# Kernel optimization log

Hardware: AMD Instinct MI355X
Metric: run time of the kernel (lower is better)

## Reference

```python
import jax, jax.numpy as jnp
import numpy as np

N = 100000   # nodes (single ntype)
R = 3        # relations
E = 500000   # edges per relation
H = 4        # attention heads
F = 64       # out_feat per head
IN = 256     # in_feat
NEG_SLOPE = 0.2  # DGL GATConv default


def setup_inputs() -> dict:
    key = jax.random.key(0)
    ks = jax.random.split(key, 7)
    x = jax.random.normal(ks[0], (N, IN), jnp.float32)
    src = jax.random.randint(ks[1], (R, E), 0, N, dtype=jnp.int32)
    dst = jax.random.randint(ks[2], (R, E), 0, N, dtype=jnp.int32)
    W = jax.random.normal(ks[3], (R, IN, H * F), jnp.float32) / np.sqrt(IN).astype(np.float32)
    attn_l = jax.random.normal(ks[4], (R, H, F), jnp.float32) * 0.1
    attn_r = jax.random.normal(ks[5], (R, H, F), jnp.float32) * 0.1
    bias = jnp.zeros((R, H * F), jnp.float32)
    return {"x": x, "W": W, "attn_l": attn_l, "attn_r": attn_r, "bias": bias,
            "src": src, "dst": dst}


def _gat_relation(x, W_r, al_r, ar_r, b_r, src_r, dst_r):
    # projection: [N, H, F]
    z = (x @ W_r).reshape(N, H, F)
    # per-node attention logits: [N, H]
    el = jnp.sum(z * al_r, axis=-1)
    er = jnp.sum(z * ar_r, axis=-1)
    # edge scores: [E, H]
    e = jax.nn.leaky_relu(el[src_r] + er[dst_r], negative_slope=NEG_SLOPE)
    # segment softmax over incoming edges of each dst node
    m = jax.ops.segment_max(e, dst_r, num_segments=N)      # [N, H]
    ee = jnp.exp(e - m[dst_r])                              # [E, H]
    den = jax.ops.segment_sum(ee, dst_r, num_segments=N)   # [N, H]
    alpha = ee / den[dst_r]                                 # [E, H]
    # weighted scatter-aggregate: [N, H, F]
    rst = jax.ops.segment_sum(z[src_r] * alpha[:, :, None], dst_r, num_segments=N)
    return rst + b_r.reshape(1, H, F)


def reference(x, W, attn_l, attn_r, bias, src, dst):
    # HeteroGraphConv aggregates relations targeting the same ntype with 'sum'
    out = jnp.zeros((N, H, F), x.dtype)
    for r in range(R):
        out = out + _gat_relation(x, W[r], attn_l[r], attn_r[r], bias[r], src[r], dst[r])
    # RelGATConvLayer._apply: activation(h.view(-1, out_feat*num_heads)); dropout=0
    return jax.nn.elu(out.reshape(N, H * F))
```

## Files before the change

### kernel.cpp

```cpp
#include <hip/hip_runtime.h>
#include <hip/hip_bf16.h>


#define RN 100000
#define RE 500000
#define RH 4
#define RIN 256
#define RR 3
#define RHF 256
#define NE3 (RR * RE)

typedef __attribute__((ext_vector_type(8))) short short8;
typedef __attribute__((ext_vector_type(4))) float f32x4;

static __device__ __forceinline__ float b2f(unsigned short u) {
  return __uint_as_float(((unsigned int)u) << 16);
}
static __device__ __forceinline__ unsigned short f2b(float f) {
  unsigned int u = __float_as_uint(f);
  u += 0x7FFF + ((u >> 16) & 1);
  return (unsigned short)(u >> 16);
}

__global__ __launch_bounds__(256) void rgat_convx(
    const float* __restrict__ x, unsigned short* __restrict__ xb) {
  const size_t i = ((size_t)blockIdx.x * 256 + threadIdx.x) * 4;
  if (i >= (size_t)RN * RIN) return;
  const float4 v = *(const float4*)(x + i);
  ushort4 o;
  o.x = f2b(v.x); o.y = f2b(v.y); o.z = f2b(v.z); o.w = f2b(v.w);
  *(ushort4*)(xb + i) = o;
}

__global__ __launch_bounds__(256) void rgat_convw(
    const float* __restrict__ W, unsigned short* __restrict__ wbt) {
  const int o = blockIdx.x * 256 + threadIdx.x;
  if (o >= RR * RIN * RHF) return;
  const int r = o / (RIN * RHF);
  const int rem = o - r * (RIN * RHF);
  const int n = rem >> 8;
  const int k = rem & 255;
  wbt[o] = f2b(W[r * (RIN * RHF) + k * RHF + n]);
}

__global__ __launch_bounds__(256) void rgat_gemm_bf16(
    const unsigned short* __restrict__ xb, const unsigned short* __restrict__ wbt,
    unsigned short* __restrict__ zb, const float* __restrict__ al,
    const float* __restrict__ ar, float* __restrict__ el,
    float* __restrict__ er) {
  __shared__ unsigned short As[128 * 32];
  __shared__ unsigned short Bs[128 * 32];
  const int tid = threadIdx.x;
  const int lane = tid & 63, wid = tid >> 6;
  const int wr = wid >> 1, wc = wid & 1;
  const int m0 = blockIdx.x * 128;
  const int n0 = blockIdx.y * 128;
  const int r  = blockIdx.z;

  f32x4 acc[4][4] = {};
  const unsigned short* Bbase = wbt + (size_t)r * (RIN * RHF);

  for (int k0 = 0; k0 < RIN; k0 += 32) {
#pragma unroll
    for (int i = 0; i < 2; ++i) {
      const int c = wid * 128 + i * 64 + lane;
      const int row = c >> 2, c4 = c & 3;
      const unsigned short* ga = xb + (size_t)(m0 + row) * RIN + k0 + c4 * 8;
      __builtin_amdgcn_global_load_lds(
          (const __attribute__((address_space(1))) void*)ga,
          (__attribute__((address_space(3))) void*)(As + (wid * 128 + i * 64) * 8),
          16, 0, 0);
      const unsigned short* gb = Bbase + (size_t)(n0 + row) * RIN + k0 + c4 * 8;
      __builtin_amdgcn_global_load_lds(
          (const __attribute__((address_space(1))) void*)gb,
          (__attribute__((address_space(3))) void*)(Bs + (wid * 128 + i * 64) * 8),
          16, 0, 0);
    }
    asm volatile("s_waitcnt vmcnt(0)" ::: "memory");
    __syncthreads();

    short8 af[4], bfr[4];
#pragma unroll
    for (int mi = 0; mi < 4; ++mi)
      af[mi] = *(const short8*)(As + ((wr * 64 + mi * 16 + (lane & 15)) * 32 + (lane >> 4) * 8));
#pragma unroll
    for (int ni = 0; ni < 4; ++ni)
      bfr[ni] = *(const short8*)(Bs + ((wc * 64 + ni * 16 + (lane & 15)) * 32 + (lane >> 4) * 8));
#pragma unroll
    for (int mi = 0; mi < 4; ++mi)
#pragma unroll
      for (int ni = 0; ni < 4; ++ni)
        acc[mi][ni] = __builtin_amdgcn_mfma_f32_16x16x32_bf16(af[mi], bfr[ni], acc[mi][ni], 0, 0, 0);
    __syncthreads();
  }

  const int head = blockIdx.y * 2 + wc;
  float alv[4], arv[4];
#pragma unroll
  for (int ni = 0; ni < 4; ++ni) {
    alv[ni] = al[r * RHF + head * 64 + ni * 16 + (lane & 15)];
    arv[ni] = ar[r * RHF + head * 64 + ni * 16 + (lane & 15)];
  }

  const int mbase = m0 + wr * 64;
#pragma unroll
  for (int mi = 0; mi < 4; ++mi) {
#pragma unroll
    for (int q = 0; q < 4; ++q) {
      const int m = mbase + mi * 16 + (lane >> 4) * 4 + q;
      float pl = 0.f, pr = 0.f;
#pragma unroll
      for (int ni = 0; ni < 4; ++ni) {
        pl += acc[mi][ni][q] * alv[ni];
        pr += acc[mi][ni][q] * arv[ni];
      }
#pragma unroll
      for (int off = 1; off < 16; off <<= 1) {
        pl += __shfl_xor(pl, off);
        pr += __shfl_xor(pr, off);
      }
      if (m < RN) {
        if ((lane & 15) == 0) {
          el[(size_t)(r * (size_t)RN + m) * RH + head] = pl;
          er[(size_t)(r * (size_t)RN + m) * RH + head] = pr;
        }
        unsigned short* zrow = zb + (size_t)r * ((size_t)RN * RHF) + (size_t)m * RHF
                               + n0 + wc * 64 + (lane & 15);
#pragma unroll
        for (int ni = 0; ni < 4; ++ni) zrow[ni * 16] = f2b(acc[mi][ni][q]);
      }
    }
  }
}

__global__ __launch_bounds__(256) void rgat_hist(
    const int* __restrict__ dst, int* __restrict__ degm) {
  const int i = blockIdx.x * 256 + threadIdx.x;
  if (i >= NE3) return;
  atomicAdd(&degm[dst[i]], 1);
}

__global__ __launch_bounds__(256) void rgat_scan1(
    const int* __restrict__ deg, int* __restrict__ offs, int* __restrict__ bsum) {
  __shared__ int sh[256];
  const int tid = threadIdx.x;
  const int base = blockIdx.x * 1024 + tid * 4;
  int v[4]; int s = 0;
#pragma unroll
  for (int j = 0; j < 4; ++j) {
    v[j] = (base + j < RN) ? deg[base + j] : 0;
    s += v[j];
  }
  sh[tid] = s;
  __syncthreads();
  for (int off = 1; off < 256; off <<= 1) {
    int t = (tid >= off) ? sh[tid - off] : 0;
    __syncthreads();
    sh[tid] += t;
    __syncthreads();
  }
  int run = sh[tid] - s;
  if (tid == 255) bsum[blockIdx.x] = sh[255];
#pragma unroll
  for (int j = 0; j < 4; ++j) {
    if (base + j < RN) offs[base + j] = run;
    run += v[j];
  }
}

__global__ __launch_bounds__(512) void rgat_scan2(int* __restrict__ bsum, int nb) {
  __shared__ int sh[512];
  const int tid = threadIdx.x;
  const int v = (tid < nb) ? bsum[tid] : 0;
  sh[tid] = v;
  __syncthreads();
  for (int off = 1; off < 512; off <<= 1) {
    int t = (tid >= off) ? sh[tid - off] : 0;
    __syncthreads();
    sh[tid] += t;
    __syncthreads();
  }
  if (tid < nb) bsum[tid] = sh[tid] - v;
}

__global__ __launch_bounds__(256) void rgat_scan3(
    int* __restrict__ offs, const int* __restrict__ bsum) {
  const int base = blockIdx.x * 1024 + threadIdx.x * 4;
  const int b = bsum[blockIdx.x];
#pragma unroll
  for (int j = 0; j < 4; ++j)
    if (base + j < RN) offs[base + j] += b;
}

__global__ __launch_bounds__(256) void rgat_scatter(
    const int* __restrict__ src, const int* __restrict__ dst,
    const float* __restrict__ el, const float* __restrict__ er,
    int* __restrict__ offsm, int* __restrict__ czoff,
    float4* __restrict__ cee) {
  const int i = blockIdx.x * 256 + threadIdx.x;
  if (i >= NE3) return;
  const int r = i / RE;
  const int s = src[i];
  const int d = dst[i];
  const int pos = atomicAdd(&offsm[d], 1);
  const float4 elv = *(const float4*)(el + (size_t)(r * (size_t)RN + s) * RH);
  const float4 erv = *(const float4*)(er + (size_t)(r * (size_t)RN + d) * RH);
  float e0 = elv.x + erv.x, e1 = elv.y + erv.y, e2 = elv.z + erv.z, e3 = elv.w + erv.w;
  e0 = e0 > 0.f ? e0 : 0.2f * e0;
  e1 = e1 > 0.f ? e1 : 0.2f * e1;
  e2 = e2 > 0.f ? e2 : 0.2f * e2;
  e3 = e3 > 0.f ? e3 : 0.2f * e3;
  czoff[pos] = r * RN + s;
  cee[pos] = make_float4(__expf(e0), __expf(e1), __expf(e2), __expf(e3));
}

__global__ __launch_bounds__(256) void rgat_aggregate(
    const unsigned short* __restrict__ zb, const int* __restrict__ czoff,
    const float4* __restrict__ cee, const int* __restrict__ degm,
    const int* __restrict__ offsm, const float* __restrict__ bias,
    float* __restrict__ out) {
  __shared__ float shn[4][RR][RHF];
  __shared__ float shd[4][RR][RH];
  const int n = blockIdx.x;
  const int wid = threadIdx.x >> 6, lane = threadIdx.x & 63;
  const int h = lane >> 4;
  const int c = lane * 4;

  const int d = degm[n];
  const int start = offsm[n] - d;

  float4 acc0 = {0.f, 0.f, 0.f, 0.f}, acc1 = acc0, acc2 = acc0;
  float den0 = 0.f, den1 = 0.f, den2 = 0.f;

  const unsigned short* zc = zb + c;

  for (int base = wid; base < d; base += 16) {
    int zo[4];
    float4 ef[4];
    ushort4 zv[4];
#pragma unroll
    for (int j = 0; j < 4; ++j) {
      const int t = base + j * 4;
      if (t < d) {
        zo[j] = czoff[start + t];
        ef[j] = cee[start + t];
      } else {
        zo[j] = -1;
      }
    }
#pragma unroll
    for (int j = 0; j < 4; ++j)
      if (zo[j] >= 0) zv[j] = *(const ushort4*)(zc + (size_t)zo[j] * RHF);
#pragma unroll
    for (int j = 0; j < 4; ++j) {
      if (zo[j] < 0) continue;
      const float a = (h == 0) ? ef[j].x : (h == 1) ? ef[j].y : (h == 2) ? ef[j].z : ef[j].w;
      const float z0 = b2f(zv[j].x), z1 = b2f(zv[j].y), z2 = b2f(zv[j].z), z3 = b2f(zv[j].w);
      if (zo[j] < RN) {
        acc0.x += a * z0; acc0.y += a * z1; acc0.z += a * z2; acc0.w += a * z3; den0 += a;
      } else if (zo[j] < 2 * RN) {
        acc1.x += a * z0; acc1.y += a * z1; acc1.z += a * z2; acc1.w += a * z3; den1 += a;
      } else {
        acc2.x += a * z0; acc2.y += a * z1; acc2.z += a * z2; acc2.w += a * z3; den2 += a;
      }
    }
  }

  *(float4*)&shn[wid][0][c] = acc0;
  *(float4*)&shn[wid][1][c] = acc1;
  *(float4*)&shn[wid][2][c] = acc2;
  if ((lane & 15) == 0) {
    shd[wid][0][h] = den0;
    shd[wid][1][h] = den1;
    shd[wid][2][h] = den2;
  }
  __syncthreads();

  const int col = threadIdx.x;
  const int hh = col >> 6;
  float v = bias[col] + bias[RHF + col] + bias[2 * RHF + col];
#pragma unroll
  for (int r = 0; r < RR; ++r) {
    const float dn = shd[0][r][hh] + shd[1][r][hh] + shd[2][r][hh] + shd[3][r][hh];
    const float nm = shn[0][r][col] + shn[1][r][col] + shn[2][r][col] + shn[3][r][col];
    v += (dn > 0.f) ? nm / dn : 0.f;
  }
  v = v > 0.f ? v : (__expf(v) - 1.f);
  out[(size_t)n * RHF + col] = v;
}

extern "C" void kernel_launch(void* const* d_in, const int* in_sizes, int n_in,
                              void* d_out, int out_size, void* d_ws, size_t ws_size,
                              hipStream_t stream) {
  const float* x    = (const float*)d_in[0];
  const float* W    = (const float*)d_in[1];
  const float* al   = (const float*)d_in[2];
  const float* ar   = (const float*)d_in[3];
  const float* bias = (const float*)d_in[4];
  const int*   src  = (const int*)d_in[5];
  const int*   dst  = (const int*)d_in[6];
  float* out = (float*)d_out;

  char* p = (char*)d_ws;
  unsigned short* xb  = (unsigned short*)p; p += (size_t)RN * RIN * 2;
  unsigned short* wbt = (unsigned short*)p; p += (size_t)RR * RIN * RHF * 2;
  unsigned short* zb  = (unsigned short*)p; p += (size_t)RR * RN * RHF * 2;
  float* el    = (float*)p;  p += (size_t)RR * RN * RH * 4;
  float* er    = (float*)p;  p += (size_t)RR * RN * RH * 4;
  int* degm    = (int*)p;    p += (size_t)RN * 4;
  int* offsm   = (int*)p;    p += (size_t)RN * 4;
  int* czoff   = (int*)p;    p += (size_t)NE3 * 4;
  float4* cee  = (float4*)p; p += (size_t)NE3 * 16;
  int* bsum    = (int*)p;    p += 2048;

  const int NB1 = (RN + 1023) / 1024;

  hipMemsetAsync(degm, 0, (size_t)RN * 4, stream);

  rgat_convx<<<(RN * RIN / 4 + 255) / 256, 256, 0, stream>>>(x, xb);
  rgat_convw<<<(RR * RIN * RHF + 255) / 256, 256, 0, stream>>>(W, wbt);

  rgat_hist<<<(NE3 + 255) / 256, 256, 0, stream>>>(dst, degm);
  rgat_scan1<<<NB1, 256, 0, stream>>>(degm, offsm, bsum);
  rgat_scan2<<<1, 512, 0, stream>>>(bsum, NB1);
  rgat_scan3<<<NB1, 256, 0, stream>>>(offsm, bsum);

  rgat_gemm_bf16<<<dim3((RN + 127) / 128, RHF / 128, RR), 256, 0, stream>>>(
      xb, wbt, zb, al, ar, el, er);

  rgat_scatter<<<(NE3 + 255) / 256, 256, 0, stream>>>(src, dst, el, er, offsm,
                                                      czoff, cee);

  rgat_aggregate<<<RN, 256, 0, stream>>>(zb, czoff, cee, degm, offsm, bias, out);
}
```

Before: 646.5 us.

## Bucket CSR edges by (dst, relation) and gather 8-wide bf16 rows per half-wave

The CSR is now keyed by (dst node, relation), so the degree histogram, scan and scatter run over N*R buckets instead of N. The aggregate kernel loops per relation without per-edge branches and stores only the source index. Each half-wave handles one edge and loads 16-byte short8 rows, which doubles the gather width per lane. The scan now covers three times as many entries (294 scan blocks, within the 512-thread scan2 limit), and the aggregate loop has less unrolled memory-level parallelism.

```diff
diff --git a/kernel.cpp b/kernel.cpp
--- a/kernel.cpp
+++ b/kernel.cpp
@@ -9,6 +9,7 @@
 #define RR 3
 #define RHF 256
 #define NE3 (RR * RE)
+#define N3  (RR * RN)
 
 typedef __attribute__((ext_vector_type(8))) short short8;
 typedef __attribute__((ext_vector_type(4))) float f32x4;
@@ -134,10 +135,11 @@
 }
 
 __global__ __launch_bounds__(256) void rgat_hist(
-    const int* __restrict__ dst, int* __restrict__ degm) {
+    const int* __restrict__ dst, int* __restrict__ deg2) {
   const int i = blockIdx.x * 256 + threadIdx.x;
   if (i >= NE3) return;
-  atomicAdd(&degm[dst[i]], 1);
+  const int r = i / RE;
+  atomicAdd(&deg2[dst[i] * RR + r], 1);
 }
 
 __global__ __launch_bounds__(256) void rgat_scan1(
@@ -148,7 +150,7 @@
   int v[4]; int s = 0;
 #pragma unroll
   for (int j = 0; j < 4; ++j) {
-    v[j] = (base + j < RN) ? deg[base + j] : 0;
+    v[j] = (base + j < N3) ? deg[base + j] : 0;
     s += v[j];
   }
   sh[tid] = s;
@@ -163,7 +165,7 @@
   if (tid == 255) bsum[blockIdx.x] = sh[255];
 #pragma unroll
   for (int j = 0; j < 4; ++j) {
-    if (base + j < RN) offs[base + j] = run;
+    if (base + j < N3) offs[base + j] = run;
     run += v[j];
   }
 }
@@ -189,20 +191,20 @@
   const int b = bsum[blockIdx.x];
 #pragma unroll
   for (int j = 0; j < 4; ++j)
-    if (base + j < RN) offs[base + j] += b;
+    if (base + j < N3) offs[base + j] += b;
 }
 
 __global__ __launch_bounds__(256) void rgat_scatter(
     const int* __restrict__ src, const int* __restrict__ dst,
     const float* __restrict__ el, const float* __restrict__ er,
-    int* __restrict__ offsm, int* __restrict__ czoff,
+    int* __restrict__ offs2, int* __restrict__ csrc,
     float4* __restrict__ cee) {
   const int i = blockIdx.x * 256 + threadIdx.x;
   if (i >= NE3) return;
   const int r = i / RE;
   const int s = src[i];
   const int d = dst[i];
-  const int pos = atomicAdd(&offsm[d], 1);
+  const int pos = atomicAdd(&offs2[d * RR + r], 1);
   const float4 elv = *(const float4*)(el + (size_t)(r * (size_t)RN + s) * RH);
   const float4 erv = *(const float4*)(er + (size_t)(r * (size_t)RN + d) * RH);
   float e0 = elv.x + erv.x, e1 = elv.y + erv.y, e2 = elv.z + erv.z, e3 = elv.w + erv.w;
@@ -210,73 +212,71 @@
   e1 = e1 > 0.f ? e1 : 0.2f * e1;
   e2 = e2 > 0.f ? e2 : 0.2f * e2;
   e3 = e3 > 0.f ? e3 : 0.2f * e3;
-  czoff[pos] = r * RN + s;
+  csrc[pos] = s;
   cee[pos] = make_float4(__expf(e0), __expf(e1), __expf(e2), __expf(e3));
 }
 
 __global__ __launch_bounds__(256) void rgat_aggregate(
-    const unsigned short* __restrict__ zb, const int* __restrict__ czoff,
-    const float4* __restrict__ cee, const int* __restrict__ degm,
-    const int* __restrict__ offsm, const float* __restrict__ bias,
+    const unsigned short* __restrict__ zb, const int* __restrict__ csrc,
+    const float* __restrict__ ceef, const int* __restrict__ deg2,
+    const int* __restrict__ offs2, const float* __restrict__ bias,
     float* __restrict__ out) {
   __shared__ float shn[4][RR][RHF];
   __shared__ float shd[4][RR][RH];
   const int n = blockIdx.x;
-  const int wid = threadIdx.x >> 6, lane = threadIdx.x & 63;
-  const int h = lane >> 4;
-  const int c = lane * 4;
-
-  const int d = degm[n];
-  const int start = offsm[n] - d;
-
-  float4 acc0 = {0.f, 0.f, 0.f, 0.f}, acc1 = acc0, acc2 = acc0;
-  float den0 = 0.f, den1 = 0.f, den2 = 0.f;
-
-  const unsigned short* zc = zb + c;
-
-  for (int base = wid; base < d; base += 16) {
-    int zo[4];
-    float4 ef[4];
-    ushort4 zv[4];
-#pragma unroll
-    for (int j = 0; j < 4; ++j) {
-      const int t = base + j * 4;
-      if (t < d) {
-        zo[j] = czoff[start + t];
-        ef[j] = cee[start + t];
-      } else {
-        zo[j] = -1;
-      }
+  const int tid = threadIdx.x;
+  const int wid = tid >> 6, lane = tid & 63;
+  const int hw = tid >> 5;
+  const int sub = lane & 31;
+  const int h = sub >> 3;
+  const int c = sub * 8;
+
+  float accr[RR][8];
+  float denr[RR];
+#pragma unroll
+  for (int r = 0; r < RR; ++r) {
+    denr[r] = 0.f;
+#pragma unroll
+    for (int k = 0; k < 8; ++k) accr[r][k] = 0.f;
+  }
+
+#pragma unroll
+  for (int r = 0; r < RR; ++r) {
+    const int key = n * RR + r;
+    const int dr = deg2[key];
+    const int end = offs2[key];
+    const int start = end - dr;
+    const unsigned short* zB = zb + (size_t)r * ((size_t)RN * RHF) + c;
+    for (int t = hw; t < dr; t += 8) {
+      const int p = start + t;
+      const int s = csrc[p];
+      const float a = ceef[p * 4 + h];
+      const short8 zv = *(const short8*)(zB + (size_t)s * RHF);
+      denr[r] += a;
+#pragma unroll
+      for (int k = 0; k < 8; ++k)
+        accr[r][k] += a * b2f((unsigned short)zv[k]);
     }
-#pragma unroll
-    for (int j = 0; j < 4; ++j)
-      if (zo[j] >= 0) zv[j] = *(const ushort4*)(zc + (size_t)zo[j] * RHF);
-#pragma unroll
-    for (int j = 0; j < 4; ++j) {
-      if (zo[j] < 0) continue;
-      const float a = (h == 0) ? ef[j].x : (h == 1) ? ef[j].y : (h == 2) ? ef[j].z : ef[j].w;
-      const float z0 = b2f(zv[j].x), z1 = b2f(zv[j].y), z2 = b2f(zv[j].z), z3 = b2f(zv[j].w);
-      if (zo[j] < RN) {
-        acc0.x += a * z0; acc0.y += a * z1; acc0.z += a * z2; acc0.w += a * z3; den0 += a;
-      } else if (zo[j] < 2 * RN) {
-        acc1.x += a * z0; acc1.y += a * z1; acc1.z += a * z2; acc1.w += a * z3; den1 += a;
-      } else {
-        acc2.x += a * z0; acc2.y += a * z1; acc2.z += a * z2; acc2.w += a * z3; den2 += a;
-      }
+  }
+
+#pragma unroll
+  for (int r = 0; r < RR; ++r) {
+    denr[r] += __shfl_xor(denr[r], 32);
+#pragma unroll
+    for (int k = 0; k < 8; ++k) accr[r][k] += __shfl_xor(accr[r][k], 32);
+  }
+
+  if (lane < 32) {
+#pragma unroll
+    for (int r = 0; r < RR; ++r) {
+      *(float4*)&shn[wid][r][c] = make_float4(accr[r][0], accr[r][1], accr[r][2], accr[r][3]);
+      *(float4*)&shn[wid][r][c + 4] = make_float4(accr[r][4], accr[r][5], accr[r][6], accr[r][7]);
+      if ((sub & 7) == 0) shd[wid][r][h] = denr[r];
     }
   }
-
-  *(float4*)&shn[wid][0][c] = acc0;
-  *(float4*)&shn[wid][1][c] = acc1;
-  *(float4*)&shn[wid][2][c] = acc2;
-  if ((lane & 15) == 0) {
-    shd[wid][0][h] = den0;
-    shd[wid][1][h] = den1;
-    shd[wid][2][h] = den2;
-  }
   __syncthreads();
 
-  const int col = threadIdx.x;
+  const int col = tid;
   const int hh = col >> 6;
   float v = bias[col] + bias[RHF + col] + bias[2 * RHF + col];
 #pragma unroll
@@ -307,29 +307,30 @@
   unsigned short* zb  = (unsigned short*)p; p += (size_t)RR * RN * RHF * 2;
   float* el    = (float*)p;  p += (size_t)RR * RN * RH * 4;
   float* er    = (float*)p;  p += (size_t)RR * RN * RH * 4;
-  int* degm    = (int*)p;    p += (size_t)RN * 4;
-  int* offsm   = (int*)p;    p += (size_t)RN * 4;
-  int* czoff   = (int*)p;    p += (size_t)NE3 * 4;
+  int* deg2    = (int*)p;    p += (size_t)N3 * 4;
+  int* offs2   = (int*)p;    p += (size_t)N3 * 4;
+  int* csrc    = (int*)p;    p += (size_t)NE3 * 4;
   float4* cee  = (float4*)p; p += (size_t)NE3 * 16;
   int* bsum    = (int*)p;    p += 2048;
 
-  const int NB1 = (RN + 1023) / 1024;
-
-  hipMemsetAsync(degm, 0, (size_t)RN * 4, stream);
+  const int NB1 = (N3 + 1023) / 1024;
+
+  hipMemsetAsync(deg2, 0, (size_t)N3 * 4, stream);
 
   rgat_convx<<<(RN * RIN / 4 + 255) / 256, 256, 0, stream>>>(x, xb);
   rgat_convw<<<(RR * RIN * RHF + 255) / 256, 256, 0, stream>>>(W, wbt);
 
-  rgat_hist<<<(NE3 + 255) / 256, 256, 0, stream>>>(dst, degm);
-  rgat_scan1<<<NB1, 256, 0, stream>>>(degm, offsm, bsum);
+  rgat_hist<<<(NE3 + 255) / 256, 256, 0, stream>>>(dst, deg2);
+  rgat_scan1<<<NB1, 256, 0, stream>>>(deg2, offs2, bsum);
   rgat_scan2<<<1, 512, 0, stream>>>(bsum, NB1);
-  rgat_scan3<<<NB1, 256, 0, stream>>>(offsm, bsum);
+  rgat_scan3<<<NB1, 256, 0, stream>>>(offs2, bsum);
 
   rgat_gemm_bf16<<<dim3((RN + 127) / 128, RHF / 128, RR), 256, 0, stream>>>(
       xb, wbt, zb, al, ar, el, er);
 
-  rgat_scatter<<<(NE3 + 255) / 256, 256, 0, stream>>>(src, dst, el, er, offsm,
-                                                      czoff, cee);
-
-  rgat_aggregate<<<RN, 256, 0, stream>>>(zb, czoff, cee, degm, offsm, bias, out);
-}
+  rgat_scatter<<<(NE3 + 255) / 256, 256, 0, stream>>>(src, dst, el, er, offs2,
+                                                      csrc, cee);
+
+  rgat_aggregate<<<RN, 256, 0, stream>>>(zb, csrc, (const float*)cee, deg2,
+                                         offs2, bias, out);
+}
```

New measurement: 677.3 us. +4.8%, slower.
